# Kernel tuning notes

Measured on AMD Instinct MI355X. Metric: run time of the kernel, lower is better.

The kernel has to match this reference:

```python
import jax, jax.numpy as jnp
import numpy as np

P = 8        # patch size
STRIDE = 4   # reference patch stride
SR = 12      # search radius
SS = 3       # search step -> 9x9 = 81 candidates
K = 16       # group size (3rd dim of 3D transform)
LAM = 2.7    # hard threshold multiplier
TWO_STEP = True


def _dct_mat(n):
    k = np.arange(n)[:, None].astype(np.float64)
    i = np.arange(n)[None, :].astype(np.float64)
    m = np.cos(np.pi * (2 * i + 1) * k / (2 * n)) * np.sqrt(2.0 / n)
    m[0] /= np.sqrt(2.0)
    return jnp.asarray(m, jnp.float32)


def _hadamard(n):
    h = np.array([[1.0]])
    while h.shape[0] < n:
        h = np.kron(h, np.array([[1.0, 1.0], [1.0, -1.0]])) / np.sqrt(2.0)
    return jnp.asarray(h, jnp.float32)

D8 = _dct_mat(P)
H16 = _hadamard(K)


def _extract_patches(img):
    # img (H, W) -> (Hp*Wp, P*P) patches at stride 1
    H, W = img.shape
    Hp, Wp = H - P + 1, W - P + 1
    cols = [img[di:di + Hp, dj:dj + Wp] for di in range(P) for dj in range(P)]
    return jnp.stack(cols, -1).reshape(Hp * Wp, P * P), Hp, Wp


def _block_match(patches, Hp, Wp):
    # returns (N, K) flat patch indices of best-matching groups
    ri = jnp.arange(0, Hp, STRIDE)
    rj = jnp.arange(0, Wp, STRIDE)
    RI, RJ = jnp.meshgrid(ri, rj, indexing='ij')
    RI, RJ = RI.reshape(-1), RJ.reshape(-1)                     # (N,)
    offs = jnp.arange(-SR, SR + 1, SS)
    OI, OJ = jnp.meshgrid(offs, offs, indexing='ij')
    ci = jnp.clip(RI[:, None] + OI.reshape(-1)[None, :], 0, Hp - 1)
    cj = jnp.clip(RJ[:, None] + OJ.reshape(-1)[None, :], 0, Wp - 1)
    cidx = ci * Wp + cj                                         # (N, C)
    cand = patches[cidx]                                        # (N, C, 64)
    ref = patches[RI * Wp + RJ]                                 # (N, 64)
    dist = (jnp.sum(cand * cand, -1)
            - 2.0 * jnp.einsum('nce,ne->nc', cand, ref)
            + jnp.sum(ref * ref, -1)[:, None])
    _, top = jax.lax.top_k(-dist, K)
    return jnp.take_along_axis(cidx, top, axis=1)               # (N, K)


def _fwd3d(groups):
    # (N, K, P*P) -> 3D transform coeffs (N, K, P, P)
    g = groups.reshape(groups.shape[0], K, P, P)
    c = jnp.einsum('ab,nkbc,dc->nkad', D8, g, D8)   # 2D DCT per patch
    return jnp.einsum('gk,nkad->ngad', H16, c)      # 1D Hadamard across group


def _inv3d(coef):
    c = jnp.einsum('gk,ngad->nkad', H16, coef)      # H^T (orthonormal)
    g = jnp.einsum('ab,nkad,dc->nkbc', D8, c, D8)   # inverse 2D DCT
    return g.reshape(coef.shape[0], K, P * P)


def _aggregate(vals, w, gidx, Hp, Wp, H, W):
    # vals (N,K,64) filtered patches, w (N,) group weights, gidx (N,K)
    gi, gj = gidx // Wp, gidx % Wp
    offs = (jnp.arange(P)[:, None] * W + jnp.arange(P)[None, :]).reshape(-1)
    pix = ((gi * W + gj)[..., None] + offs).reshape(-1)         # (N*K*64,)
    wv = jnp.broadcast_to(w[:, None, None], vals.shape)
    num = jnp.zeros(H * W, jnp.float32).at[pix].add((wv * vals).reshape(-1))
    den = jnp.zeros(H * W, jnp.float32).at[pix].add(wv.reshape(-1))
    return (num / jnp.maximum(den, 1e-8)).reshape(H, W)


def _bm3d_channel(img, sigma2):
    H, W = img.shape
    sigma2 = jnp.float32(sigma2)
    sigma = jnp.sqrt(sigma2)
    patches, Hp, Wp = _extract_patches(img)

    # ---- step 1: hard-threshold collaborative filtering ----
    gidx = _block_match(patches, Hp, Wp)
    groups = patches[gidx]                                      # (N,K,64)
    coef = _fwd3d(groups)
    mask = (jnp.abs(coef) > LAM * sigma)
    mask = mask.at[:, 0, 0, 0].set(True)                        # keep DC
    coef_ht = jnp.where(mask, coef, 0.0)
    nnz = jnp.sum(mask.astype(jnp.float32), axis=(1, 2, 3))
    w_ht = 1.0 / (sigma2 * jnp.maximum(nnz, 1.0))
    basic = _aggregate(_inv3d(coef_ht), w_ht, gidx, Hp, Wp, H, W)
    if not TWO_STEP:
        return basic

    # ---- step 2: Wiener filtering using the basic estimate ----
    patches_b, _, _ = _extract_patches(basic)
    gidx2 = _block_match(patches_b, Hp, Wp)
    cb = _fwd3d(patches_b[gidx2])                               # basic coeffs
    cn = _fwd3d(patches[gidx2])                                 # noisy coeffs
    wien = cb * cb / (cb * cb + sigma2)
    coef_w = wien * cn
    w_wie = 1.0 / (sigma2 * jnp.maximum(jnp.sum(wien * wien, axis=(1, 2, 3)), 1e-8))
    return _aggregate(_inv3d(coef_w), w_wie, gidx2, Hp, Wp, H, W)


def setup_inputs() -> dict:
    key = jax.random.key(0)
    im = jax.random.randint(key, (1, 1, 384, 384), 0, 256, dtype=jnp.int32)
    return {"im": im, "variance": 25}


def reference(im, variance):
    # im: (1, 1, H, W) int tensor, values >= 0; variance: scalar noise variance
    outs = [_bm3d_channel(im[0, c].astype(jnp.float32), variance)
            for c in range(im.shape[1])]
    return jnp.stack(outs, 0)[None]                             # (1, C, H, W) float32
```

## Files before the change

kernel.cpp:

```cpp
#include <hip/hip_runtime.h>
#include <math.h>

#define TS 44
#define FINF 3.4e38f

__device__ __forceinline__ int iclip(int v, int hi) {
  return v < 0 ? 0 : (v > hi ? hi : v);
}

constexpr float CA = 0.35355339059327373f;
constexpr float K1 = 0.49039264020161522f;
constexpr float K2 = 0.46193976625564337f;
constexpr float K3 = 0.41573480615127262f;
constexpr float K4 = 0.35355339059327379f;
constexpr float K5 = 0.27778511650980111f;
constexpr float K6 = 0.19134171618254489f;
constexpr float K7 = 0.097545161008064135f;

constexpr float DCT8[8][8] = {
  { CA, CA, CA, CA, CA, CA, CA, CA},
  { K1, K3, K5, K7,-K7,-K5,-K3,-K1},
  { K2, K6,-K6,-K2,-K2,-K6, K6, K2},
  { K3,-K7,-K1,-K5, K5, K1, K7,-K3},
  { K4,-K4,-K4, K4, K4,-K4,-K4, K4},
  { K5,-K1, K7, K3,-K3,-K7, K1,-K5},
  { K6,-K2, K2,-K6,-K6, K2,-K2, K6},
  { K7,-K5, K3,-K1, K1,-K3, K5,-K7},
};

__device__ __forceinline__ int sxor_i(int v, int m) {
  switch (m) {
    case 1:  return __builtin_amdgcn_update_dpp(0, v, 0xB1, 0xF, 0xF, true);
    case 2:  return __builtin_amdgcn_update_dpp(0, v, 0x4E, 0xF, 0xF, true);
    case 4:  return __builtin_amdgcn_ds_swizzle(v, (4 << 10) | 0x1F);
    case 8:  return __builtin_amdgcn_ds_swizzle(v, (8 << 10) | 0x1F);
    case 16: return __builtin_amdgcn_ds_swizzle(v, (16 << 10) | 0x1F);
    default: return __shfl_xor(v, 32, 64);
  }
}
__device__ __forceinline__ float sxor_f(float v, int m) {
  return __int_as_float(sxor_i(__float_as_int(v), m));
}

__device__ __forceinline__ float qbcast(float v, int s) {
  int x = __float_as_int(v), r;
  switch (s) {
    case 0:  r = __builtin_amdgcn_update_dpp(0, x, 0x00, 0xF, 0xF, true); break;
    case 1:  r = __builtin_amdgcn_update_dpp(0, x, 0x55, 0xF, 0xF, true); break;
    case 2:  r = __builtin_amdgcn_update_dpp(0, x, 0xAA, 0xF, 0xF, true); break;
    default: r = __builtin_amdgcn_update_dpp(0, x, 0xFF, 0xF, 0xF, true); break;
  }
  return __int_as_float(r);
}

__device__ __forceinline__ void fwd_rowcol(float X[2][8], float U[2][8],
                                           const float Ca0[8], const float Ca1[8]) {
#pragma unroll
  for (int r = 0; r < 2; r++)
#pragma unroll
    for (int d = 0; d < 8; d++) {
      float s = X[r][0] * DCT8[d][0];
#pragma unroll
      for (int c = 1; c < 8; c++) s += X[r][c] * DCT8[d][c];
      U[r][d] = s;
    }
#pragma unroll
  for (int r = 0; r < 2; r++)
#pragma unroll
    for (int d = 0; d < 8; d++) X[r][d] = 0.f;
#pragma unroll
  for (int b = 0; b < 8; b++)
#pragma unroll
    for (int d = 0; d < 8; d++) {
      float yb = qbcast(U[b & 1][d], b >> 1);
      X[0][d] += Ca0[b] * yb;
      X[1][d] += Ca1[b] * yb;
    }
}

__device__ __forceinline__ void inv_colrow(float X[2][8], float U[2][8],
                                           const float Ct0[8], const float Ct1[8]) {
#pragma unroll
  for (int r = 0; r < 2; r++)
#pragma unroll
    for (int d = 0; d < 8; d++) U[r][d] = 0.f;
#pragma unroll
  for (int a = 0; a < 8; a++)
#pragma unroll
    for (int d = 0; d < 8; d++) {
      float za = qbcast(X[a & 1][d], a >> 1);
      U[0][d] += Ct0[a] * za;
      U[1][d] += Ct1[a] * za;
    }
#pragma unroll
  for (int r = 0; r < 2; r++)
#pragma unroll
    for (int c = 0; c < 8; c++) {
      float s = U[r][0] * DCT8[0][c];
#pragma unroll
      for (int d = 1; d < 8; d++) s += U[r][d] * DCT8[d][c];
      X[r][c] = s;
    }
}

__device__ __forceinline__ void had16r(float X[2][8], int lane) {
#pragma unroll
  for (int m = 4; m <= 32; m <<= 1) {
    bool hi = (lane & m) != 0;
#pragma unroll
    for (int r = 0; r < 2; r++)
#pragma unroll
      for (int d = 0; d < 8; d++) {
        float tv = sxor_f(X[r][d], m);
        X[r][d] = hi ? (tv - X[r][d]) : (X[r][d] + tv);
      }
  }
#pragma unroll
  for (int r = 0; r < 2; r++)
#pragma unroll
    for (int d = 0; d < 8; d++) X[r][d] *= 0.25f;
}

template <int WIEN>
__global__ __launch_bounds__(256, 8) void bm3d_pass(
    const int* __restrict__ img, const float* __restrict__ basic,
    const int* __restrict__ pvar,
    float* __restrict__ num, float* __restrict__ den) {
  __shared__ float ldsD[64];
  __shared__ float bufA[32 * TS];
  __shared__ float bufB[32 * TS];

  int t = threadIdx.x;
  int brow = blockIdx.x / 24, bcb = blockIdx.x - brow * 24;
  int ri = brow * 4;
  int bim = ri - 12;       int bi = bim < 0 ? 0 : (bim > 352 ? 352 : bim);
  int ubm = 16 * bcb - 12; int ub = ubm < 0 ? 0 : (ubm > 352 ? 352 : ubm);

  if (t < 64) ldsD[t] = DCT8[t >> 3][t & 7];

  for (int e4 = t; e4 < 32 * 11; e4 += 256) {
    int r = e4 / 11, c4 = (e4 - r * 11) << 2;
    int col = ub + c4;
    int gidx = (bi + r) * 384 + col;
    int o = r * TS + c4;
    if (col + 3 < 384) {
      int4 iv = *(const int4*)&img[gidx];
      float4 fv = make_float4((float)iv.x, (float)iv.y, (float)iv.z, (float)iv.w);
      if (WIEN) {
        *(float4*)&bufA[o] = *(const float4*)&basic[gidx];
        *(float4*)&bufB[o] = fv;
      } else {
        *(float4*)&bufA[o] = fv;
      }
    } else {
#pragma unroll
      for (int u = 0; u < 4; u++) {
        bool ok = (col + u) < 384;
        float fi = ok ? (float)img[gidx + u] : 0.f;
        if (WIEN) {
          bufA[o + u] = ok ? basic[gidx + u] : 0.f;
          bufB[o + u] = fi;
        } else {
          bufA[o + u] = fi;
        }
      }
    }
  }
  __syncthreads();

  float sigma2 = (float)pvar[0];
  int wv = t >> 6, lane = t & 63;
  int gc = bcb * 4 + wv;
  bool active = gc < 95;

  float X[2][8];
  float w = 0.f;
  int gi0 = 0, gj0 = 0;

  if (active) {
    int rj = gc * 4;
    const float* tileS = bufA;
    const float* tileN = WIEN ? bufB : bufA;

    int cB = lane < 17 ? 64 + lane : 80;
    int aiA = iclip(ri + (lane / 9) * 3 - 12, 376) - bi;
    int ajA = iclip(rj + (lane % 9) * 3 - 12, 376) - ub;
    int aiB = iclip(ri + (cB / 9) * 3 - 12, 376) - bi;
    int ajB = iclip(rj + (cB % 9) * 3 - 12, 376) - ub;
    int roi = ri - bi, roj = rj - ub;
    float sccA = 0.f, scrA = 0.f, sccB = 0.f, scrB = 0.f, srr = 0.f;
#pragma unroll
    for (int i = 0; i < 8; i++) {
      const float* rr = tileS + (roi + i) * TS + roj;
      const float* ar = tileS + (aiA + i) * TS + ajA;
      const float* br = tileS + (aiB + i) * TS + ajB;
#pragma unroll
      for (int j = 0; j < 8; j++) {
        float rv = rr[j], av = ar[j], bv = br[j];
        sccA += av * av; scrA += av * rv;
        sccB += bv * bv; scrB += bv * rv;
        srr  += rv * rv;
      }
    }
    float d0 = sccA - 2.f * scrA + srr; int i0 = lane;
    float d1 = lane < 17 ? (sccB - 2.f * scrB + srr) : FINF; int i1 = 64 + lane;

    int k = lane >> 2, q = lane & 3;
    int msi = 0, msj = 0;
#pragma unroll 1
    for (int r = 0; r < 16; r++) {
      float d = d0; int i = i0;
      if (d1 < d0) { d = d1; i = i1; }
#pragma unroll
      for (int m = 1; m <= 32; m <<= 1) {
        float dd = sxor_f(d, m); int ii = sxor_i(i, m);
        if (dd < d || (dd == d && ii < i)) { d = dd; i = ii; }
      }
      if (r == k) {
        msi = iclip(ri + (i / 9) * 3 - 12, 376) - bi;
        msj = iclip(rj + (i % 9) * 3 - 12, 376) - ub;
      }
      if (i == i0) d0 = FINF;
      if (i == i1) d1 = FINF;
    }

    float Ca0[8], Ca1[8];
#pragma unroll
    for (int b = 0; b < 8; b++) {
      Ca0[b] = ldsD[(2 * q) * 8 + b];
      Ca1[b] = ldsD[(2 * q + 1) * 8 + b];
    }
    gi0 = msi + 2 * q; gj0 = msj;

    float U[2][8], ZB[2][8];

    if (WIEN) {
#pragma unroll
      for (int r = 0; r < 2; r++)
#pragma unroll
        for (int c = 0; c < 8; c++) ZB[r][c] = tileS[(gi0 + r) * TS + gj0 + c];
      fwd_rowcol(ZB, U, Ca0, Ca1);
      had16r(ZB, lane);
    }

#pragma unroll
    for (int r = 0; r < 2; r++)
#pragma unroll
      for (int c = 0; c < 8; c++) X[r][c] = tileN[(gi0 + r) * TS + gj0 + c];
    fwd_rowcol(X, U, Ca0, Ca1);
    had16r(X, lane);

    if (WIEN) {
      float part = 0.f;
#pragma unroll
      for (int r = 0; r < 2; r++)
#pragma unroll
        for (int d = 0; d < 8; d++) {
          float cb = ZB[r][d];
          float we = cb * cb / (cb * cb + sigma2);
          X[r][d] = we * X[r][d];
          part += we * we;
        }
#pragma unroll
      for (int m = 1; m <= 32; m <<= 1) part += sxor_f(part, m);
      w = 1.f / (sigma2 * fmaxf(part, 1e-8f));
    } else {
      float thr = 2.7f * sqrtf(sigma2);
      int cnt = 0;
#pragma unroll
      for (int r = 0; r < 2; r++)
#pragma unroll
        for (int d = 0; d < 8; d++) {
          bool keep = (fabsf(X[r][d]) > thr) || (lane == 0 && r == 0 && d == 0);
          cnt += (int)__popcll(__ballot(keep));
          if (!keep) X[r][d] = 0.f;
        }
      w = 1.f / (sigma2 * fmaxf((float)cnt, 1.f));
    }

    had16r(X, lane);
#pragma unroll
    for (int a = 0; a < 8; a++) {
      Ca0[a] = ldsD[a * 8 + 2 * q];
      Ca1[a] = ldsD[a * 8 + 2 * q + 1];
    }
    inv_colrow(X, U, Ca0, Ca1);
  }

  __syncthreads();
  for (int e = t; e < 32 * TS; e += 256) { bufA[e] = 0.f; bufB[e] = 0.f; }
  __syncthreads();

  if (active) {
#pragma unroll
    for (int r = 0; r < 2; r++)
#pragma unroll
      for (int c = 0; c < 8; c++) {
        int off = (gi0 + r) * TS + gj0 + c;
        atomicAdd(&bufA[off], w * X[r][c]);
        atomicAdd(&bufB[off], w);
      }
  }
  __syncthreads();

  for (int e = t; e < 32 * TS; e += 256) {
    float dv = bufB[e];
    if (dv != 0.f) {
      int r = e / TS, c = e - r * TS;
      int gp = (bi + r) * 384 + ub + c;
      atomicAdd(&num[gp], bufA[e]);
      atomicAdd(&den[gp], dv);
    }
  }
}

__global__ void div_kernel(const float* __restrict__ num,
                           const float* __restrict__ den,
                           float* __restrict__ out, int npix) {
  int i = blockIdx.x * blockDim.x + threadIdx.x;
  if (i < npix) out[i] = num[i] / fmaxf(den[i], 1e-8f);
}

extern "C" void kernel_launch(void* const* d_in, const int* in_sizes, int n_in,
                              void* d_out, int out_size, void* d_ws, size_t ws_size,
                              hipStream_t stream) {
  const int* img  = (const int*)d_in[0];
  const int* pvar = (const int*)d_in[1];
  float* out = (float*)d_out;
  float* ws  = (float*)d_ws;

  const int NPIX = 384 * 384;
  float* num1  = ws + 0 * NPIX;
  float* den1  = ws + 1 * NPIX;
  float* basic = ws + 2 * NPIX;
  float* num2  = ws + 3 * NPIX;
  float* den2  = ws + 4 * NPIX;

  hipMemsetAsync(num1, 0, (size_t)2 * NPIX * sizeof(float), stream);
  hipMemsetAsync(num2, 0, (size_t)2 * NPIX * sizeof(float), stream);

  const int NBLK = 95 * 24;
  bm3d_pass<0><<<NBLK, 256, 0, stream>>>(img, nullptr, pvar, num1, den1);
  div_kernel<<<(NPIX + 255) / 256, 256, 0, stream>>>(num1, den1, basic, NPIX);
  bm3d_pass<1><<<NBLK, 256, 0, stream>>>(img, basic, pvar, num2, den2);
  div_kernel<<<(NPIX + 255) / 256, 256, 0, stream>>>(num2, den2, out, NPIX);
}
```

Baseline: 307.8 us.

## Widen tiles to 8 waves per block and replace shuffle top-k with rank selection

Each block now handles 8 reference columns (512 threads) over a 60-wide shared tile, which cuts the halo overhead per reference and lets the loads drop their edge-guard branches. The 16-round butterfly-shuffle top-k is replaced by a rank count: every lane compares its distance against all 81 candidates stored in shared memory and writes its position into a selection slot if its rank is below 16. This trades shuffle rounds for shared-memory reads and adds two block-wide barriers. Occupancy drops to 2 blocks of 512 threads per CU, and inactive waves now compute on a duplicated column.

```diff
diff --git a/kernel.cpp b/kernel.cpp
--- a/kernel.cpp
+++ b/kernel.cpp
@@ -1,7 +1,7 @@
 #include <hip/hip_runtime.h>
 #include <math.h>
 
-#define TS 44
+#define TS 60
 #define FINF 3.4e38f
 
 __device__ __forceinline__ int iclip(int v, int hi) {
@@ -122,173 +122,155 @@
 }
 
 template <int WIEN>
-__global__ __launch_bounds__(256, 8) void bm3d_pass(
+__global__ __launch_bounds__(512, 2) void bm3d_pass(
     const int* __restrict__ img, const float* __restrict__ basic,
     const int* __restrict__ pvar,
     float* __restrict__ num, float* __restrict__ den) {
   __shared__ float ldsD[64];
+  __shared__ float wdist[8][81];
+  __shared__ int   wsel[8][16];
   __shared__ float bufA[32 * TS];
   __shared__ float bufB[32 * TS];
 
   int t = threadIdx.x;
-  int brow = blockIdx.x / 24, bcb = blockIdx.x - brow * 24;
+  int brow = blockIdx.x / 12, bcb = blockIdx.x - brow * 12;
   int ri = brow * 4;
   int bim = ri - 12;       int bi = bim < 0 ? 0 : (bim > 352 ? 352 : bim);
-  int ubm = 16 * bcb - 12; int ub = ubm < 0 ? 0 : (ubm > 352 ? 352 : ubm);
+  int ubm = 32 * bcb - 12; int ub = ubm < 0 ? 0 : (ubm > 324 ? 324 : ubm);
 
   if (t < 64) ldsD[t] = DCT8[t >> 3][t & 7];
 
-  for (int e4 = t; e4 < 32 * 11; e4 += 256) {
-    int r = e4 / 11, c4 = (e4 - r * 11) << 2;
-    int col = ub + c4;
-    int gidx = (bi + r) * 384 + col;
+  if (t < 480) {
+    int r = t / 15, c4 = (t - r * 15) << 2;
+    int gidx = (bi + r) * 384 + ub + c4;
     int o = r * TS + c4;
-    if (col + 3 < 384) {
-      int4 iv = *(const int4*)&img[gidx];
-      float4 fv = make_float4((float)iv.x, (float)iv.y, (float)iv.z, (float)iv.w);
-      if (WIEN) {
-        *(float4*)&bufA[o] = *(const float4*)&basic[gidx];
-        *(float4*)&bufB[o] = fv;
-      } else {
-        *(float4*)&bufA[o] = fv;
-      }
+    int4 iv = *(const int4*)&img[gidx];
+    float4 fv = make_float4((float)iv.x, (float)iv.y, (float)iv.z, (float)iv.w);
+    if (WIEN) {
+      *(float4*)&bufA[o] = *(const float4*)&basic[gidx];
+      *(float4*)&bufB[o] = fv;
     } else {
-#pragma unroll
-      for (int u = 0; u < 4; u++) {
-        bool ok = (col + u) < 384;
-        float fi = ok ? (float)img[gidx + u] : 0.f;
-        if (WIEN) {
-          bufA[o + u] = ok ? basic[gidx + u] : 0.f;
-          bufB[o + u] = fi;
-        } else {
-          bufA[o + u] = fi;
-        }
-      }
+      *(float4*)&bufA[o] = fv;
     }
   }
   __syncthreads();
 
   float sigma2 = (float)pvar[0];
   int wv = t >> 6, lane = t & 63;
-  int gc = bcb * 4 + wv;
+  int gc = bcb * 8 + wv;
   bool active = gc < 95;
-
-  float X[2][8];
-  float w = 0.f;
-  int gi0 = 0, gj0 = 0;
-
-  if (active) {
-    int rj = gc * 4;
-    const float* tileS = bufA;
-    const float* tileN = WIEN ? bufB : bufA;
-
-    int cB = lane < 17 ? 64 + lane : 80;
-    int aiA = iclip(ri + (lane / 9) * 3 - 12, 376) - bi;
-    int ajA = iclip(rj + (lane % 9) * 3 - 12, 376) - ub;
-    int aiB = iclip(ri + (cB / 9) * 3 - 12, 376) - bi;
-    int ajB = iclip(rj + (cB % 9) * 3 - 12, 376) - ub;
-    int roi = ri - bi, roj = rj - ub;
-    float sccA = 0.f, scrA = 0.f, sccB = 0.f, scrB = 0.f, srr = 0.f;
-#pragma unroll
-    for (int i = 0; i < 8; i++) {
-      const float* rr = tileS + (roi + i) * TS + roj;
-      const float* ar = tileS + (aiA + i) * TS + ajA;
-      const float* br = tileS + (aiB + i) * TS + ajB;
-#pragma unroll
-      for (int j = 0; j < 8; j++) {
-        float rv = rr[j], av = ar[j], bv = br[j];
-        sccA += av * av; scrA += av * rv;
-        sccB += bv * bv; scrB += bv * rv;
-        srr  += rv * rv;
+  int gcw = active ? gc : 94;
+  int rj = gcw * 4;
+
+  const float* tileS = bufA;
+  const float* tileN = WIEN ? bufB : bufA;
+
+  int cB = lane < 17 ? 64 + lane : 80;
+  int ai0 = iclip(ri + (lane / 9) * 3 - 12, 376) - bi;
+  int aj0 = iclip(rj + (lane % 9) * 3 - 12, 376) - ub;
+  int ai1 = iclip(ri + (cB / 9) * 3 - 12, 376) - bi;
+  int aj1 = iclip(rj + (cB % 9) * 3 - 12, 376) - ub;
+  int roi = ri - bi, roj = rj - ub;
+  float scc0 = 0.f, scr0 = 0.f, scc1 = 0.f, scr1 = 0.f, srr = 0.f;
+#pragma unroll
+  for (int i = 0; i < 8; i++) {
+    const float* rr = tileS + (roi + i) * TS + roj;
+    const float* ar = tileS + (ai0 + i) * TS + aj0;
+    const float* br = tileS + (ai1 + i) * TS + aj1;
+#pragma unroll
+    for (int j = 0; j < 8; j++) {
+      float rv = rr[j], av = ar[j], bv = br[j];
+      scc0 += av * av; scr0 += av * rv;
+      scc1 += bv * bv; scr1 += bv * rv;
+      srr  += rv * rv;
+    }
+  }
+  float d0 = scc0 - 2.f * scr0 + srr;
+  float d1 = lane < 17 ? (scc1 - 2.f * scr1 + srr) : FINF;
+
+  wdist[wv][lane] = d0;
+  if (lane < 17) wdist[wv][64 + lane] = d1;
+  __syncthreads();
+
+  int rank0 = 0, rank1 = 0;
+#pragma unroll 3
+  for (int c2 = 0; c2 < 81; c2++) {
+    float dd = wdist[wv][c2];
+    rank0 += (dd < d0) || (dd == d0 && c2 < lane) ? 1 : 0;
+    rank1 += (dd < d1) || (dd == d1 && c2 < 64 + lane) ? 1 : 0;
+  }
+  if (rank0 < 16) wsel[wv][rank0] = (ai0 << 8) | aj0;
+  if (lane < 17 && rank1 < 16) wsel[wv][rank1] = (ai1 << 8) | aj1;
+  __syncthreads();
+
+  int k = lane >> 2, q = lane & 3;
+  int sp = wsel[wv][k];
+  int gi0 = (sp >> 8) + 2 * q, gj0 = sp & 255;
+
+  float Ca0[8], Ca1[8];
+#pragma unroll
+  for (int b = 0; b < 8; b++) {
+    Ca0[b] = ldsD[(2 * q) * 8 + b];
+    Ca1[b] = ldsD[(2 * q + 1) * 8 + b];
+  }
+
+  float X[2][8], U[2][8], ZB[2][8];
+  float w;
+
+  if (WIEN) {
+#pragma unroll
+    for (int r = 0; r < 2; r++)
+#pragma unroll
+      for (int c = 0; c < 8; c++) ZB[r][c] = tileS[(gi0 + r) * TS + gj0 + c];
+    fwd_rowcol(ZB, U, Ca0, Ca1);
+    had16r(ZB, lane);
+  }
+
+#pragma unroll
+  for (int r = 0; r < 2; r++)
+#pragma unroll
+    for (int c = 0; c < 8; c++) X[r][c] = tileN[(gi0 + r) * TS + gj0 + c];
+  fwd_rowcol(X, U, Ca0, Ca1);
+  had16r(X, lane);
+
+  if (WIEN) {
+    float part = 0.f;
+#pragma unroll
+    for (int r = 0; r < 2; r++)
+#pragma unroll
+      for (int d = 0; d < 8; d++) {
+        float cb = ZB[r][d];
+        float we = cb * cb / (cb * cb + sigma2);
+        X[r][d] = we * X[r][d];
+        part += we * we;
       }
-    }
-    float d0 = sccA - 2.f * scrA + srr; int i0 = lane;
-    float d1 = lane < 17 ? (sccB - 2.f * scrB + srr) : FINF; int i1 = 64 + lane;
-
-    int k = lane >> 2, q = lane & 3;
-    int msi = 0, msj = 0;
-#pragma unroll 1
-    for (int r = 0; r < 16; r++) {
-      float d = d0; int i = i0;
-      if (d1 < d0) { d = d1; i = i1; }
-#pragma unroll
-      for (int m = 1; m <= 32; m <<= 1) {
-        float dd = sxor_f(d, m); int ii = sxor_i(i, m);
-        if (dd < d || (dd == d && ii < i)) { d = dd; i = ii; }
+#pragma unroll
+    for (int m = 1; m <= 32; m <<= 1) part += sxor_f(part, m);
+    w = 1.f / (sigma2 * fmaxf(part, 1e-8f));
+  } else {
+    float thr = 2.7f * sqrtf(sigma2);
+    int cnt = 0;
+#pragma unroll
+    for (int r = 0; r < 2; r++)
+#pragma unroll
+      for (int d = 0; d < 8; d++) {
+        bool keep = (fabsf(X[r][d]) > thr) || (lane == 0 && r == 0 && d == 0);
+        cnt += (int)__popcll(__ballot(keep));
+        if (!keep) X[r][d] = 0.f;
       }
-      if (r == k) {
-        msi = iclip(ri + (i / 9) * 3 - 12, 376) - bi;
-        msj = iclip(rj + (i % 9) * 3 - 12, 376) - ub;
-      }
-      if (i == i0) d0 = FINF;
-      if (i == i1) d1 = FINF;
-    }
-
-    float Ca0[8], Ca1[8];
-#pragma unroll
-    for (int b = 0; b < 8; b++) {
-      Ca0[b] = ldsD[(2 * q) * 8 + b];
-      Ca1[b] = ldsD[(2 * q + 1) * 8 + b];
-    }
-    gi0 = msi + 2 * q; gj0 = msj;
-
-    float U[2][8], ZB[2][8];
-
-    if (WIEN) {
-#pragma unroll
-      for (int r = 0; r < 2; r++)
-#pragma unroll
-        for (int c = 0; c < 8; c++) ZB[r][c] = tileS[(gi0 + r) * TS + gj0 + c];
-      fwd_rowcol(ZB, U, Ca0, Ca1);
-      had16r(ZB, lane);
-    }
-
-#pragma unroll
-    for (int r = 0; r < 2; r++)
-#pragma unroll
-      for (int c = 0; c < 8; c++) X[r][c] = tileN[(gi0 + r) * TS + gj0 + c];
-    fwd_rowcol(X, U, Ca0, Ca1);
-    had16r(X, lane);
-
-    if (WIEN) {
-      float part = 0.f;
-#pragma unroll
-      for (int r = 0; r < 2; r++)
-#pragma unroll
-        for (int d = 0; d < 8; d++) {
-          float cb = ZB[r][d];
-          float we = cb * cb / (cb * cb + sigma2);
-          X[r][d] = we * X[r][d];
-          part += we * we;
-        }
-#pragma unroll
-      for (int m = 1; m <= 32; m <<= 1) part += sxor_f(part, m);
-      w = 1.f / (sigma2 * fmaxf(part, 1e-8f));
-    } else {
-      float thr = 2.7f * sqrtf(sigma2);
-      int cnt = 0;
-#pragma unroll
-      for (int r = 0; r < 2; r++)
-#pragma unroll
-        for (int d = 0; d < 8; d++) {
-          bool keep = (fabsf(X[r][d]) > thr) || (lane == 0 && r == 0 && d == 0);
-          cnt += (int)__popcll(__ballot(keep));
-          if (!keep) X[r][d] = 0.f;
-        }
-      w = 1.f / (sigma2 * fmaxf((float)cnt, 1.f));
-    }
-
-    had16r(X, lane);
-#pragma unroll
-    for (int a = 0; a < 8; a++) {
-      Ca0[a] = ldsD[a * 8 + 2 * q];
-      Ca1[a] = ldsD[a * 8 + 2 * q + 1];
-    }
-    inv_colrow(X, U, Ca0, Ca1);
-  }
-
-  __syncthreads();
-  for (int e = t; e < 32 * TS; e += 256) { bufA[e] = 0.f; bufB[e] = 0.f; }
+    w = 1.f / (sigma2 * fmaxf((float)cnt, 1.f));
+  }
+
+  had16r(X, lane);
+#pragma unroll
+  for (int a = 0; a < 8; a++) {
+    Ca0[a] = ldsD[a * 8 + 2 * q];
+    Ca1[a] = ldsD[a * 8 + 2 * q + 1];
+  }
+  inv_colrow(X, U, Ca0, Ca1);
+
+  __syncthreads();
+  for (int e = t; e < 32 * TS; e += 512) { bufA[e] = 0.f; bufB[e] = 0.f; }
   __syncthreads();
 
   if (active) {
@@ -303,7 +285,7 @@
   }
   __syncthreads();
 
-  for (int e = t; e < 32 * TS; e += 256) {
+  for (int e = t; e < 32 * TS; e += 512) {
     float dv = bufB[e];
     if (dv != 0.f) {
       int r = e / TS, c = e - r * TS;
@@ -339,9 +321,9 @@
   hipMemsetAsync(num1, 0, (size_t)2 * NPIX * sizeof(float), stream);
   hipMemsetAsync(num2, 0, (size_t)2 * NPIX * sizeof(float), stream);
 
-  const int NBLK = 95 * 24;
-  bm3d_pass<0><<<NBLK, 256, 0, stream>>>(img, nullptr, pvar, num1, den1);
+  const int NBLK = 95 * 12;
+  bm3d_pass<0><<<NBLK, 512, 0, stream>>>(img, nullptr, pvar, num1, den1);
   div_kernel<<<(NPIX + 255) / 256, 256, 0, stream>>>(num1, den1, basic, NPIX);
-  bm3d_pass<1><<<NBLK, 256, 0, stream>>>(img, basic, pvar, num2, den2);
+  bm3d_pass<1><<<NBLK, 512, 0, stream>>>(img, basic, pvar, num2, den2);
   div_kernel<<<(NPIX + 255) / 256, 256, 0, stream>>>(num2, den2, out, NPIX);
 }
```

Measured after the change: 324.6 us. +5.5%, slower.

## Replace shuffle top-k with LDS rank selection and precompute patch energies

Applied to the files above, without the earlier changes.

Block matching no longer recomputes each candidate's squared norm. It reads them from a box-filtered table of 8x8 window energies built once per block in shared memory. Top-16 selection changes from 16 rounds of wave-wide shuffle argmin to one pass where each candidate counts how many others beat it and writes itself into a selection slot. The change also pads the tile stride to 48, loads the transposed DCT matrix from LDS with float4 reads, uses DPP for the xor-8 shuffle, and lowers launch bounds occupancy to 4. The extra LDS use and the looser occupancy bound may reduce waves per CU.

```diff
diff --git a/kernel.cpp b/kernel.cpp
--- a/kernel.cpp
+++ b/kernel.cpp
@@ -1,7 +1,7 @@
 #include <hip/hip_runtime.h>
 #include <math.h>
 
-#define TS 44
+#define TS 48
 #define FINF 3.4e38f
 
 __device__ __forceinline__ int iclip(int v, int hi) {
@@ -33,7 +33,7 @@
     case 1:  return __builtin_amdgcn_update_dpp(0, v, 0xB1, 0xF, 0xF, true);
     case 2:  return __builtin_amdgcn_update_dpp(0, v, 0x4E, 0xF, 0xF, true);
     case 4:  return __builtin_amdgcn_ds_swizzle(v, (4 << 10) | 0x1F);
-    case 8:  return __builtin_amdgcn_ds_swizzle(v, (8 << 10) | 0x1F);
+    case 8:  return __builtin_amdgcn_update_dpp(0, v, 0x128, 0xF, 0xF, true);
     case 16: return __builtin_amdgcn_ds_swizzle(v, (16 << 10) | 0x1F);
     default: return __shfl_xor(v, 32, 64);
   }
@@ -122,11 +122,15 @@
 }
 
 template <int WIEN>
-__global__ __launch_bounds__(256, 8) void bm3d_pass(
+__global__ __launch_bounds__(256, 4) void bm3d_pass(
     const int* __restrict__ img, const float* __restrict__ basic,
     const int* __restrict__ pvar,
     float* __restrict__ num, float* __restrict__ den) {
-  __shared__ float ldsD[64];
+  __shared__ float ldsD[64], ldsDT[64];
+  __shared__ __align__(16) float wdist[4][84];
+  __shared__ int wsel[4][16];
+  __shared__ float Rws[32 * 40];
+  __shared__ float S2[25 * 40];
   __shared__ float bufA[32 * TS];
   __shared__ float bufB[32 * TS];
 
@@ -137,8 +141,9 @@
   int ubm = 16 * bcb - 12; int ub = ubm < 0 ? 0 : (ubm > 352 ? 352 : ubm);
 
   if (t < 64) ldsD[t] = DCT8[t >> 3][t & 7];
-
-  for (int e4 = t; e4 < 32 * 11; e4 += 256) {
+  else if (t < 128) { int u = t - 64; ldsDT[u] = DCT8[u & 7][u >> 3]; }
+
+  for (int e4 = t; e4 < 352; e4 += 256) {
     int r = e4 / 11, c4 = (e4 - r * 11) << 2;
     int col = ub + c4;
     int gidx = (bi + r) * 384 + col;
@@ -168,80 +173,100 @@
   }
   __syncthreads();
 
+  for (int e = t; e < 32 * 37; e += 256) {
+    int r = e / 37, j = e - r * 37;
+    const float* p = bufA + r * TS + j;
+    float s = 0.f;
+#pragma unroll
+    for (int d = 0; d < 8; d++) { float v = p[d]; s += v * v; }
+    Rws[r * 40 + j] = s;
+  }
+  __syncthreads();
+  for (int e = t; e < 25 * 37; e += 256) {
+    int i = e / 37, j = e - i * 37;
+    float s = 0.f;
+#pragma unroll
+    for (int d = 0; d < 8; d++) s += Rws[(i + d) * 40 + j];
+    S2[i * 40 + j] = s;
+  }
+  __syncthreads();
+
   float sigma2 = (float)pvar[0];
   int wv = t >> 6, lane = t & 63;
   int gc = bcb * 4 + wv;
   bool active = gc < 95;
-
-  float X[2][8];
-  float w = 0.f;
-  int gi0 = 0, gj0 = 0;
-
-  if (active) {
-    int rj = gc * 4;
-    const float* tileS = bufA;
-    const float* tileN = WIEN ? bufB : bufA;
-
-    int cB = lane < 17 ? 64 + lane : 80;
-    int aiA = iclip(ri + (lane / 9) * 3 - 12, 376) - bi;
-    int ajA = iclip(rj + (lane % 9) * 3 - 12, 376) - ub;
-    int aiB = iclip(ri + (cB / 9) * 3 - 12, 376) - bi;
-    int ajB = iclip(rj + (cB % 9) * 3 - 12, 376) - ub;
-    int roi = ri - bi, roj = rj - ub;
-    float sccA = 0.f, scrA = 0.f, sccB = 0.f, scrB = 0.f, srr = 0.f;
-#pragma unroll
-    for (int i = 0; i < 8; i++) {
-      const float* rr = tileS + (roi + i) * TS + roj;
-      const float* ar = tileS + (aiA + i) * TS + ajA;
-      const float* br = tileS + (aiB + i) * TS + ajB;
-#pragma unroll
-      for (int j = 0; j < 8; j++) {
-        float rv = rr[j], av = ar[j], bv = br[j];
-        sccA += av * av; scrA += av * rv;
-        sccB += bv * bv; scrB += bv * rv;
-        srr  += rv * rv;
-      }
-    }
-    float d0 = sccA - 2.f * scrA + srr; int i0 = lane;
-    float d1 = lane < 17 ? (sccB - 2.f * scrB + srr) : FINF; int i1 = 64 + lane;
-
-    int k = lane >> 2, q = lane & 3;
-    int msi = 0, msj = 0;
-#pragma unroll 1
-    for (int r = 0; r < 16; r++) {
-      float d = d0; int i = i0;
-      if (d1 < d0) { d = d1; i = i1; }
-#pragma unroll
-      for (int m = 1; m <= 32; m <<= 1) {
-        float dd = sxor_f(d, m); int ii = sxor_i(i, m);
-        if (dd < d || (dd == d && ii < i)) { d = dd; i = ii; }
-      }
-      if (r == k) {
-        msi = iclip(ri + (i / 9) * 3 - 12, 376) - bi;
-        msj = iclip(rj + (i % 9) * 3 - 12, 376) - ub;
-      }
-      if (i == i0) d0 = FINF;
-      if (i == i1) d1 = FINF;
-    }
-
-    float Ca0[8], Ca1[8];
-#pragma unroll
-    for (int b = 0; b < 8; b++) {
-      Ca0[b] = ldsD[(2 * q) * 8 + b];
-      Ca1[b] = ldsD[(2 * q + 1) * 8 + b];
-    }
-    gi0 = msi + 2 * q; gj0 = msj;
-
-    float U[2][8], ZB[2][8];
-
-    if (WIEN) {
-#pragma unroll
-      for (int r = 0; r < 2; r++)
-#pragma unroll
-        for (int c = 0; c < 8; c++) ZB[r][c] = tileS[(gi0 + r) * TS + gj0 + c];
-      fwd_rowcol(ZB, U, Ca0, Ca1);
-      had16r(ZB, lane);
-    }
+  int rj = (active ? gc : 94) * 4;
+
+  const float* tileS = bufA;
+  const float* tileN = WIEN ? bufB : bufA;
+
+  int cB = lane < 17 ? 64 + lane : 80;
+  int aiA = iclip(ri + (lane / 9) * 3 - 12, 376) - bi;
+  int ajA = iclip(rj + (lane % 9) * 3 - 12, 376) - ub;
+  int aiB = iclip(ri + (cB / 9) * 3 - 12, 376) - bi;
+  int ajB = iclip(rj + (cB % 9) * 3 - 12, 376) - ub;
+  int roi = ri - bi, roj = rj - ub;
+
+  float scrA = 0.f, scrB = 0.f;
+#pragma unroll
+  for (int i = 0; i < 8; i++) {
+    float4 ra = *(const float4*)(tileS + (roi + i) * TS + roj);
+    float4 rb = *(const float4*)(tileS + (roi + i) * TS + roj + 4);
+    float rv[8] = {ra.x, ra.y, ra.z, ra.w, rb.x, rb.y, rb.z, rb.w};
+    const float* ap = tileS + (aiA + i) * TS + ajA;
+    const float* bp = tileS + (aiB + i) * TS + ajB;
+#pragma unroll
+    for (int j = 0; j < 8; j++) {
+      scrA += ap[j] * rv[j];
+      scrB += bp[j] * rv[j];
+    }
+  }
+  float srr = S2[roi * 40 + roj];
+  float dA = fmaf(-2.f, scrA, S2[aiA * 40 + ajA]) + srr;
+  float dB = lane < 17 ? fmaf(-2.f, scrB, S2[aiB * 40 + ajB]) + srr : FINF;
+
+  wdist[wv][lane] = dA;
+  if (lane < 17)      wdist[wv][64 + lane] = dB;
+  else if (lane < 20) wdist[wv][64 + lane] = FINF;
+
+  int rA = 0, rB = 0;
+  const float4* wp = (const float4*)&wdist[wv][0];
+  int idxB = 64 + lane;
+#pragma unroll 3
+  for (int c4 = 0; c4 < 21; c4++) {
+    float4 v = wp[c4];
+    float ev[4] = {v.x, v.y, v.z, v.w};
+#pragma unroll
+    for (int u = 0; u < 4; u++) {
+      int c2 = c4 * 4 + u;
+      rA += (ev[u] < dA || (ev[u] == dA && c2 < lane)) ? 1 : 0;
+      rB += (ev[u] < dB || (ev[u] == dB && c2 < idxB)) ? 1 : 0;
+    }
+  }
+  if (rA < 16) wsel[wv][rA] = (aiA << 8) | ajA;
+  if (lane < 17 && rB < 16) wsel[wv][rB] = (aiB << 8) | ajB;
+
+  int k = lane >> 2, q = lane & 3;
+  int sp = wsel[wv][k];
+  int gi0 = (sp >> 8) + 2 * q, gj0 = sp & 255;
+
+  float Ca0[8], Ca1[8];
+  *(float4*)&Ca0[0] = *(const float4*)&ldsD[(2 * q) * 8];
+  *(float4*)&Ca0[4] = *(const float4*)&ldsD[(2 * q) * 8 + 4];
+  *(float4*)&Ca1[0] = *(const float4*)&ldsD[(2 * q + 1) * 8];
+  *(float4*)&Ca1[4] = *(const float4*)&ldsD[(2 * q + 1) * 8 + 4];
+
+  float X[2][8], U[2][8];
+  float w;
+
+  if (WIEN) {
+    float Z[2][8];
+#pragma unroll
+    for (int r = 0; r < 2; r++)
+#pragma unroll
+      for (int c = 0; c < 8; c++) Z[r][c] = tileS[(gi0 + r) * TS + gj0 + c];
+    fwd_rowcol(Z, U, Ca0, Ca1);
+    had16r(Z, lane);
 
 #pragma unroll
     for (int r = 0; r < 2; r++)
@@ -250,42 +275,47 @@
     fwd_rowcol(X, U, Ca0, Ca1);
     had16r(X, lane);
 
-    if (WIEN) {
-      float part = 0.f;
-#pragma unroll
-      for (int r = 0; r < 2; r++)
-#pragma unroll
-        for (int d = 0; d < 8; d++) {
-          float cb = ZB[r][d];
-          float we = cb * cb / (cb * cb + sigma2);
-          X[r][d] = we * X[r][d];
-          part += we * we;
-        }
-#pragma unroll
-      for (int m = 1; m <= 32; m <<= 1) part += sxor_f(part, m);
-      w = 1.f / (sigma2 * fmaxf(part, 1e-8f));
-    } else {
-      float thr = 2.7f * sqrtf(sigma2);
-      int cnt = 0;
-#pragma unroll
-      for (int r = 0; r < 2; r++)
-#pragma unroll
-        for (int d = 0; d < 8; d++) {
-          bool keep = (fabsf(X[r][d]) > thr) || (lane == 0 && r == 0 && d == 0);
-          cnt += (int)__popcll(__ballot(keep));
-          if (!keep) X[r][d] = 0.f;
-        }
-      w = 1.f / (sigma2 * fmaxf((float)cnt, 1.f));
-    }
-
+    float p = 0.f;
+#pragma unroll
+    for (int r = 0; r < 2; r++)
+#pragma unroll
+      for (int d = 0; d < 8; d++) {
+        float cb = Z[r][d];
+        float we = cb * cb / (cb * cb + sigma2);
+        X[r][d] = we * X[r][d];
+        p += we * we;
+      }
+#pragma unroll
+    for (int m = 1; m <= 32; m <<= 1) p += sxor_f(p, m);
+    w = 1.f / (sigma2 * fmaxf(p, 1e-8f));
+  } else {
+#pragma unroll
+    for (int r = 0; r < 2; r++)
+#pragma unroll
+      for (int c = 0; c < 8; c++) X[r][c] = tileN[(gi0 + r) * TS + gj0 + c];
+    fwd_rowcol(X, U, Ca0, Ca1);
     had16r(X, lane);
-#pragma unroll
-    for (int a = 0; a < 8; a++) {
-      Ca0[a] = ldsD[a * 8 + 2 * q];
-      Ca1[a] = ldsD[a * 8 + 2 * q + 1];
-    }
-    inv_colrow(X, U, Ca0, Ca1);
-  }
+
+    float thr = 2.7f * sqrtf(sigma2);
+    int cnt = 0;
+#pragma unroll
+    for (int r = 0; r < 2; r++)
+#pragma unroll
+      for (int d = 0; d < 8; d++) {
+        bool keep = (fabsf(X[r][d]) > thr) || (lane == 0 && r == 0 && d == 0);
+        cnt += (int)__popcll(__ballot(keep));
+        if (!keep) X[r][d] = 0.f;
+      }
+    w = 1.f / (sigma2 * fmaxf((float)cnt, 1.f));
+  }
+
+  had16r(X, lane);
+#pragma unroll
+  for (int a = 0; a < 8; a++) {
+    Ca0[a] = ldsDT[(2 * q) * 8 + a];
+    Ca1[a] = ldsDT[(2 * q + 1) * 8 + a];
+  }
+  inv_colrow(X, U, Ca0, Ca1);
 
   __syncthreads();
   for (int e = t; e < 32 * TS; e += 256) { bufA[e] = 0.f; bufB[e] = 0.f; }
```

New measurement: 314.2 us. 2.1% more time.
